# Performance work log

Hardware: AMD Instinct MI355X
Metric: run time of the kernel (lower is better)

## Reference

```python
import jax, jax.numpy as jnp
import numpy as np

NUM_EXPERTS = 64
TOP_K = 2
AUX_COEF = 0.01
Z_COEF = 0.001
INIT_STD = 0.02


def setup_inputs() -> dict:
    key = jax.random.key(0)
    k1, k2 = jax.random.split(key)
    B, S, D = 4, 4096, 2048
    x = jax.random.normal(k1, (B, S, D), dtype=jnp.float32)
    gate_w = jax.random.normal(k2, (NUM_EXPERTS, D), dtype=jnp.float32) * INIT_STD
    return {"x": x, "gate_w": gate_w}


def reference(x, gate_w):
    B, S, D = x.shape
    E, K = NUM_EXPERTS, TOP_K
    # gate linear: (B,S,D) @ (D,E) -> (B,S,E), cast to fp32 like .float()
    logits = jnp.einsum('bsd,ed->bse', x, gate_w).astype(jnp.float32)
    weights = jax.nn.softmax(logits, axis=-1)
    top_weights, top_indices = jax.lax.top_k(weights, K)
    top_weights = top_weights / jnp.sum(top_weights, axis=-1, keepdims=True)
    # load-balance aux loss (training branch)
    flat_idx = top_indices.reshape(-1)
    tokens_per_expert = jax.ops.segment_sum(
        jnp.ones_like(flat_idx, dtype=jnp.float32), flat_idx, num_segments=E)
    f = tokens_per_expert / (B * S * K)
    P = jnp.mean(weights, axis=(0, 1))
    balance_loss = E * jnp.sum(f * P)
    z_loss = jnp.mean(jnp.square(jax.nn.logsumexp(logits, axis=-1)))
    aux_loss = AUX_COEF * balance_loss + Z_COEF * z_loss
    return top_indices, top_weights, aux_loss
```

## Files before the change

kernel.cpp:

```cpp
#include <hip/hip_runtime.h>
#include <math.h>

#define NTOK 16384
#define DDIM 2048
#define NEXP 64
#define MTILE 32
#define KSUP 128
#define NSUP 16

typedef __attribute__((ext_vector_type(8))) short bf16x8;
typedef __attribute__((ext_vector_type(4))) float f32x4;

__device__ __forceinline__ unsigned short f2bf(float f) {
    unsigned int u = __builtin_bit_cast(unsigned int, f);
    u += 0x7fffu + ((u >> 16) & 1u);
    return (unsigned short)(u >> 16);
}
__device__ __forceinline__ float bf2f(unsigned short s) {
    return __builtin_bit_cast(float, ((unsigned int)s) << 16);
}
__device__ __forceinline__ void split3(float x, unsigned short &h,
                                       unsigned short &m, unsigned short &l) {
    h = f2bf(x);
    float r1 = x - bf2f(h);
    m = f2bf(r1);
    float r2 = r1 - bf2f(m);
    l = f2bf(r2);
}

__global__ void k_wpack(const float* __restrict__ gw, unsigned short* __restrict__ wp) {
    int idx = blockIdx.x * 256 + threadIdx.x;
    int lane = idx & 63;
    int ks   = (idx >> 6) & 63;
    int eg   = idx >> 12;
    int e  = eg * 16 + (lane & 15);
    int k0 = ks * 32 + (lane >> 4) * 8;
    const float* src = gw + (size_t)e * DDIM + k0;
    union { unsigned short s[8]; uint4 v; } H, M, L;
    #pragma unroll
    for (int j = 0; j < 8; ++j) split3(src[j], H.s[j], M.s[j], L.s[j]);
    size_t fb = (size_t)(eg * 64 + ks) * 1536 + lane * 8;
    *(uint4*)(wp + fb)        = H.v;
    *(uint4*)(wp + fb + 512)  = M.v;
    *(uint4*)(wp + fb + 1024) = L.v;
}

__global__ __launch_bounds__(256, 4)
void k_main(const float* __restrict__ x, const unsigned short* __restrict__ wp,
            float* __restrict__ out, float* __restrict__ gcnt,
            float* __restrict__ gP, float* __restrict__ gz) {
    __shared__ __align__(16) char As[24576];
    __shared__ float Lg[MTILE][65];
    __shared__ float Ps[NEXP], Cnt[NEXP], Zs;

    const int tid = threadIdx.x;
    if (tid < NEXP) { Ps[tid] = 0.f; Cnt[tid] = 0.f; }
    if (tid == 0) Zs = 0.f;

    const int tok0 = blockIdx.x * MTILE;
    const int lane = tid & 63;
    const int eg   = __builtin_amdgcn_readfirstlane(tid >> 6);

    const int subk = tid & 31;
    const int tokq = tid >> 5;
    const float* xbase = x + (size_t)(tok0 + tokq) * DDIM + subk * 4;

    float4 cur0 = *(const float4*)(xbase);
    float4 cur1 = *(const float4*)(xbase + 8 * DDIM);
    float4 cur2 = *(const float4*)(xbase + 16 * DDIM);
    float4 cur3 = *(const float4*)(xbase + 24 * DDIM);

    f32x4 acc0 = {0.f, 0.f, 0.f, 0.f};
    f32x4 acc1 = {0.f, 0.f, 0.f, 0.f};

    const int tau   = lane & 15;
    const int kappa = lane >> 4;

    const unsigned short* wpe = wp + (size_t)eg * 64 * 1536 + lane * 8;
    bf16x8 wf[2][3];
    #pragma unroll
    for (int p = 0; p < 3; ++p) wf[0][p] = *(const bf16x8*)(wpe + p * 512);
    #pragma unroll
    for (int p = 0; p < 3; ++p) wf[1][p] = *(const bf16x8*)(wpe + 1536 + p * 512);

    for (int ss = 0; ss < NSUP; ++ss) {
        char* bb = As;
        {
            float4 v[4] = {cur0, cur1, cur2, cur3};
            #pragma unroll
            for (int r = 0; r < 4; ++r) {
                int row = tokq + 8 * r;
                unsigned short h0,h1,h2,h3, m0,m1,m2,m3, l0,l1,l2,l3;
                split3(v[r].x, h0, m0, l0);
                split3(v[r].y, h1, m1, l1);
                split3(v[r].z, h2, m2, l2);
                split3(v[r].w, h3, m3, l3);
                uint2 H = make_uint2((unsigned)h0 | ((unsigned)h1 << 16),
                                     (unsigned)h2 | ((unsigned)h3 << 16));
                uint2 M = make_uint2((unsigned)m0 | ((unsigned)m1 << 16),
                                     (unsigned)m2 | ((unsigned)m3 << 16));
                uint2 L = make_uint2((unsigned)l0 | ((unsigned)l1 << 16),
                                     (unsigned)l2 | ((unsigned)l3 << 16));
                char* pb = bb + row * 256 + (((subk >> 1) ^ (row & 15)) << 4)
                              + (subk & 1) * 8;
                *(uint2*)(pb)         = H;
                *(uint2*)(pb + 8192)  = M;
                *(uint2*)(pb + 16384) = L;
            }
        }
        if (ss + 1 < NSUP) {
            const float* nb = xbase + (ss + 1) * KSUP;
            cur0 = *(const float4*)(nb);
            cur1 = *(const float4*)(nb + 8 * DDIM);
            cur2 = *(const float4*)(nb + 16 * DDIM);
            cur3 = *(const float4*)(nb + 24 * DDIM);
        }
        __syncthreads();
        #pragma unroll
        for (int ks = 0; ks < 4; ++ks) {
            int slotr = ((ks * 4 + kappa) ^ tau) << 4;
            const char* p0 = bb + tau * 256 + slotr;
            const char* p1 = bb + (16 + tau) * 256 + slotr;
            bf16x8 Ah0 = *(const bf16x8*)(p0);
            bf16x8 Am0 = *(const bf16x8*)(p0 + 8192);
            bf16x8 Al0 = *(const bf16x8*)(p0 + 16384);
            bf16x8 Ah1 = *(const bf16x8*)(p1);
            bf16x8 Am1 = *(const bf16x8*)(p1 + 8192);
            bf16x8 Al1 = *(const bf16x8*)(p1 + 16384);
            bf16x8 Bh = wf[ks & 1][0];
            bf16x8 Bm = wf[ks & 1][1];
            bf16x8 Bl = wf[ks & 1][2];

            acc0 = __builtin_amdgcn_mfma_f32_16x16x32_bf16(Ah0, Bh, acc0, 0, 0, 0);
            acc0 = __builtin_amdgcn_mfma_f32_16x16x32_bf16(Ah0, Bm, acc0, 0, 0, 0);
            acc0 = __builtin_amdgcn_mfma_f32_16x16x32_bf16(Am0, Bh, acc0, 0, 0, 0);
            acc0 = __builtin_amdgcn_mfma_f32_16x16x32_bf16(Ah0, Bl, acc0, 0, 0, 0);
            acc0 = __builtin_amdgcn_mfma_f32_16x16x32_bf16(Al0, Bh, acc0, 0, 0, 0);
            acc0 = __builtin_amdgcn_mfma_f32_16x16x32_bf16(Am0, Bm, acc0, 0, 0, 0);

            acc1 = __builtin_amdgcn_mfma_f32_16x16x32_bf16(Ah1, Bh, acc1, 0, 0, 0);
            acc1 = __builtin_amdgcn_mfma_f32_16x16x32_bf16(Ah1, Bm, acc1, 0, 0, 0);
            acc1 = __builtin_amdgcn_mfma_f32_16x16x32_bf16(Am1, Bh, acc1, 0, 0, 0);
            acc1 = __builtin_amdgcn_mfma_f32_16x16x32_bf16(Ah1, Bl, acc1, 0, 0, 0);
            acc1 = __builtin_amdgcn_mfma_f32_16x16x32_bf16(Al1, Bh, acc1, 0, 0, 0);
            acc1 = __builtin_amdgcn_mfma_f32_16x16x32_bf16(Am1, Bm, acc1, 0, 0, 0);

            int nk = ((ss << 2) + ks + 2) & 63;
            #pragma unroll
            for (int pI = 0; pI < 3; ++pI)
                wf[ks & 1][pI] = *(const bf16x8*)(wpe + (size_t)nk * 1536 + pI * 512);
        }
        __syncthreads();
    }

    #pragma unroll
    for (int j = 0; j < 4; ++j) {
        Lg[kappa * 4 + j][eg * 16 + tau]      = acc0[j];
        Lg[16 + kappa * 4 + j][eg * 16 + tau] = acc1[j];
    }
    __syncthreads();

    float Pacc = 0.f, zacc = 0.f;
    const int wv = tid >> 6;
    for (int i = 0; i < 8; ++i) {
        int t = wv * 8 + i;
        float l = Lg[t][lane];
        float mx = l;
        #pragma unroll
        for (int off = 32; off > 0; off >>= 1) mx = fmaxf(mx, __shfl_xor(mx, off));
        float s = expf(l - mx);
        float sum = s;
        #pragma unroll
        for (int off = 32; off > 0; off >>= 1) sum += __shfl_xor(sum, off);
        Pacc += s / sum;

        unsigned long long b1 = __ballot(l == mx);
        int i1 = __ffsll(b1) - 1;
        float l2 = (lane == i1) ? -INFINITY : l;
        float m2 = l2;
        #pragma unroll
        for (int off = 32; off > 0; off >>= 1) m2 = fmaxf(m2, __shfl_xor(m2, off));
        unsigned long long b2 = __ballot(l2 == m2);
        int i2 = __ffsll(b2) - 1;

        if (lane == 0) {
            float s2  = expf(m2 - mx);
            float inv = 1.f / (1.f + s2);
            int gt = tok0 + t;
            ((float2*)out)[gt]              = make_float2((float)i1, (float)i2);
            ((float2*)(out + 2 * NTOK))[gt] = make_float2(inv, s2 * inv);
            atomicAdd(&Cnt[i1], 1.f);
            atomicAdd(&Cnt[i2], 1.f);
            float lse = mx + logf(sum);
            zacc += lse * lse;
        }
    }
    atomicAdd(&Ps[lane], Pacc);
    if (lane == 0) atomicAdd(&Zs, zacc);
    __syncthreads();

    if (tid < NEXP) {
        atomicAdd(&gcnt[tid], Cnt[tid]);
        atomicAdd(&gP[tid],   Ps[tid]);
    }
    if (tid == 0) atomicAdd(gz, Zs);
}

__global__ void k_final(const float* __restrict__ ws, float* __restrict__ out) {
    int lane = threadIdx.x;
    float v = ws[lane] * ws[64 + lane];
    #pragma unroll
    for (int off = 32; off > 0; off >>= 1) v += __shfl_xor(v, off);
    if (lane == 0) {
        float bal = 64.f * v / (32768.f * 16384.f);
        float z   = ws[128] / 16384.f;
        out[4 * NTOK] = 0.01f * bal + 0.001f * z;
    }
}

extern "C" void kernel_launch(void* const* d_in, const int* in_sizes, int n_in,
                              void* d_out, int out_size, void* d_ws, size_t ws_size,
                              hipStream_t stream) {
    const float* x  = (const float*)d_in[0];
    const float* gw = (const float*)d_in[1];
    float* out = (float*)d_out;
    float* wsf = (float*)d_ws;
    unsigned short* wp = (unsigned short*)((char*)d_ws + 1024);

    hipMemsetAsync(d_ws, 0, 516, stream);
    k_wpack<<<64, 256, 0, stream>>>(gw, wp);
    k_main<<<NTOK / MTILE, 256, 0, stream>>>(x, wp, out, wsf, wsf + 64, wsf + 128);
    k_final<<<1, 64, 0, stream>>>(wsf, out);
}
```

Before: 84.22 us.

## Halve token tile and double-buffer split-bf16 A staging in LDS

Shrinks the per-block token tile from 32 to 16 rows, which doubles the grid size, and replaces the single LDS buffer with a double buffer. Staging the next K-chunk now overlaps with MFMA work on the current one, so only one barrier per iteration is needed instead of two. In exchange, each block reloads the full packed gate weights for only half as many tokens, which doubles weight traffic from L2, and there is less MFMA work per LDS load.

After: 86.55 us. 1.03x slower.

```diff
diff --git a/kernel.cpp b/kernel.cpp
--- a/kernel.cpp
+++ b/kernel.cpp
@@ -4,7 +4,7 @@
 #define NTOK 16384
 #define DDIM 2048
 #define NEXP 64
-#define MTILE 32
+#define MTILE 16
 #define KSUP 128
 #define NSUP 16
 
@@ -45,11 +45,27 @@
     *(uint4*)(wp + fb + 1024) = L.v;
 }
 
+__device__ __forceinline__ void stage4(char* bb, int srow, int subk, int c, float4 v) {
+    unsigned short h0,h1,h2,h3, m0,m1,m2,m3, l0,l1,l2,l3;
+    split3(v.x, h0, m0, l0);
+    split3(v.y, h1, m1, l1);
+    split3(v.z, h2, m2, l2);
+    split3(v.w, h3, m3, l3);
+    char* pb = bb + srow * 256 + (((c * 8 + (subk >> 1)) ^ srow) << 4)
+                  + (subk & 1) * 8;
+    *(uint2*)(pb)        = make_uint2((unsigned)h0 | ((unsigned)h1 << 16),
+                                      (unsigned)h2 | ((unsigned)h3 << 16));
+    *(uint2*)(pb + 4096) = make_uint2((unsigned)m0 | ((unsigned)m1 << 16),
+                                      (unsigned)m2 | ((unsigned)m3 << 16));
+    *(uint2*)(pb + 8192) = make_uint2((unsigned)l0 | ((unsigned)l1 << 16),
+                                      (unsigned)l2 | ((unsigned)l3 << 16));
+}
+
 __global__ __launch_bounds__(256, 4)
 void k_main(const float* __restrict__ x, const unsigned short* __restrict__ wp,
             float* __restrict__ out, float* __restrict__ gcnt,
             float* __restrict__ gP, float* __restrict__ gz) {
-    __shared__ __align__(16) char As[24576];
+    __shared__ __align__(16) char As[2][12288];
     __shared__ float Lg[MTILE][65];
     __shared__ float Ps[NEXP], Cnt[NEXP], Zs;
 
@@ -60,21 +76,19 @@
     const int tok0 = blockIdx.x * MTILE;
     const int lane = tid & 63;
     const int eg   = __builtin_amdgcn_readfirstlane(tid >> 6);
-
-    const int subk = tid & 31;
-    const int tokq = tid >> 5;
-    const float* xbase = x + (size_t)(tok0 + tokq) * DDIM + subk * 4;
-
-    float4 cur0 = *(const float4*)(xbase);
-    float4 cur1 = *(const float4*)(xbase + 8 * DDIM);
-    float4 cur2 = *(const float4*)(xbase + 16 * DDIM);
-    float4 cur3 = *(const float4*)(xbase + 24 * DDIM);
-
-    f32x4 acc0 = {0.f, 0.f, 0.f, 0.f};
-    f32x4 acc1 = {0.f, 0.f, 0.f, 0.f};
-
-    const int tau   = lane & 15;
+    const int tau  = lane & 15;
     const int kappa = lane >> 4;
+
+    const int srow = tid >> 4;
+    const int subk = tid & 15;
+    const float* xb = x + (size_t)(tok0 + srow) * DDIM + subk * 4;
+
+    float4 xc0 = *(const float4*)(xb);
+    float4 xc1 = *(const float4*)(xb + 64);
+    stage4(As[0], srow, subk, 0, xc0);
+    stage4(As[0], srow, subk, 1, xc1);
+    xc0 = *(const float4*)(xb + 128);
+    xc1 = *(const float4*)(xb + 128 + 64);
 
     const unsigned short* wpe = wp + (size_t)eg * 64 * 1536 + lane * 8;
     bf16x8 wf[2][3];
@@ -83,87 +97,52 @@
     #pragma unroll
     for (int p = 0; p < 3; ++p) wf[1][p] = *(const bf16x8*)(wpe + 1536 + p * 512);
 
+    f32x4 acc = {0.f, 0.f, 0.f, 0.f};
+
     for (int ss = 0; ss < NSUP; ++ss) {
-        char* bb = As;
-        {
-            float4 v[4] = {cur0, cur1, cur2, cur3};
-            #pragma unroll
-            for (int r = 0; r < 4; ++r) {
-                int row = tokq + 8 * r;
-                unsigned short h0,h1,h2,h3, m0,m1,m2,m3, l0,l1,l2,l3;
-                split3(v[r].x, h0, m0, l0);
-                split3(v[r].y, h1, m1, l1);
-                split3(v[r].z, h2, m2, l2);
-                split3(v[r].w, h3, m3, l3);
-                uint2 H = make_uint2((unsigned)h0 | ((unsigned)h1 << 16),
-                                     (unsigned)h2 | ((unsigned)h3 << 16));
-                uint2 M = make_uint2((unsigned)m0 | ((unsigned)m1 << 16),
-                                     (unsigned)m2 | ((unsigned)m3 << 16));
-                uint2 L = make_uint2((unsigned)l0 | ((unsigned)l1 << 16),
-                                     (unsigned)l2 | ((unsigned)l3 << 16));
-                char* pb = bb + row * 256 + (((subk >> 1) ^ (row & 15)) << 4)
-                              + (subk & 1) * 8;
-                *(uint2*)(pb)         = H;
-                *(uint2*)(pb + 8192)  = M;
-                *(uint2*)(pb + 16384) = L;
-            }
+        __syncthreads();
+        if (ss + 1 < NSUP) {
+            char* nb = As[(ss + 1) & 1];
+            stage4(nb, srow, subk, 0, xc0);
+            stage4(nb, srow, subk, 1, xc1);
+            int nss = (ss + 2) & (NSUP - 1);
+            xc0 = *(const float4*)(xb + nss * KSUP);
+            xc1 = *(const float4*)(xb + nss * KSUP + 64);
         }
-        if (ss + 1 < NSUP) {
-            const float* nb = xbase + (ss + 1) * KSUP;
-            cur0 = *(const float4*)(nb);
-            cur1 = *(const float4*)(nb + 8 * DDIM);
-            cur2 = *(const float4*)(nb + 16 * DDIM);
-            cur3 = *(const float4*)(nb + 24 * DDIM);
-        }
-        __syncthreads();
+        const char* bb = As[ss & 1];
         #pragma unroll
         for (int ks = 0; ks < 4; ++ks) {
-            int slotr = ((ks * 4 + kappa) ^ tau) << 4;
-            const char* p0 = bb + tau * 256 + slotr;
-            const char* p1 = bb + (16 + tau) * 256 + slotr;
-            bf16x8 Ah0 = *(const bf16x8*)(p0);
-            bf16x8 Am0 = *(const bf16x8*)(p0 + 8192);
-            bf16x8 Al0 = *(const bf16x8*)(p0 + 16384);
-            bf16x8 Ah1 = *(const bf16x8*)(p1);
-            bf16x8 Am1 = *(const bf16x8*)(p1 + 8192);
-            bf16x8 Al1 = *(const bf16x8*)(p1 + 16384);
+            const char* p0 = bb + tau * 256 + ((((ks << 2) + kappa) ^ tau) << 4);
+            bf16x8 Ah = *(const bf16x8*)(p0);
+            bf16x8 Am = *(const bf16x8*)(p0 + 4096);
+            bf16x8 Al = *(const bf16x8*)(p0 + 8192);
             bf16x8 Bh = wf[ks & 1][0];
             bf16x8 Bm = wf[ks & 1][1];
             bf16x8 Bl = wf[ks & 1][2];
 
-            acc0 = __builtin_amdgcn_mfma_f32_16x16x32_bf16(Ah0, Bh, acc0, 0, 0, 0);
-            acc0 = __builtin_amdgcn_mfma_f32_16x16x32_bf16(Ah0, Bm, acc0, 0, 0, 0);
-            acc0 = __builtin_amdgcn_mfma_f32_16x16x32_bf16(Am0, Bh, acc0, 0, 0, 0);
-            acc0 = __builtin_amdgcn_mfma_f32_16x16x32_bf16(Ah0, Bl, acc0, 0, 0, 0);
-            acc0 = __builtin_amdgcn_mfma_f32_16x16x32_bf16(Al0, Bh, acc0, 0, 0, 0);
-            acc0 = __builtin_amdgcn_mfma_f32_16x16x32_bf16(Am0, Bm, acc0, 0, 0, 0);
-
-            acc1 = __builtin_amdgcn_mfma_f32_16x16x32_bf16(Ah1, Bh, acc1, 0, 0, 0);
-            acc1 = __builtin_amdgcn_mfma_f32_16x16x32_bf16(Ah1, Bm, acc1, 0, 0, 0);
-            acc1 = __builtin_amdgcn_mfma_f32_16x16x32_bf16(Am1, Bh, acc1, 0, 0, 0);
-            acc1 = __builtin_amdgcn_mfma_f32_16x16x32_bf16(Ah1, Bl, acc1, 0, 0, 0);
-            acc1 = __builtin_amdgcn_mfma_f32_16x16x32_bf16(Al1, Bh, acc1, 0, 0, 0);
-            acc1 = __builtin_amdgcn_mfma_f32_16x16x32_bf16(Am1, Bm, acc1, 0, 0, 0);
+            acc = __builtin_amdgcn_mfma_f32_16x16x32_bf16(Ah, Bh, acc, 0, 0, 0);
+            acc = __builtin_amdgcn_mfma_f32_16x16x32_bf16(Ah, Bm, acc, 0, 0, 0);
+            acc = __builtin_amdgcn_mfma_f32_16x16x32_bf16(Am, Bh, acc, 0, 0, 0);
+            acc = __builtin_amdgcn_mfma_f32_16x16x32_bf16(Ah, Bl, acc, 0, 0, 0);
+            acc = __builtin_amdgcn_mfma_f32_16x16x32_bf16(Al, Bh, acc, 0, 0, 0);
+            acc = __builtin_amdgcn_mfma_f32_16x16x32_bf16(Am, Bm, acc, 0, 0, 0);
 
             int nk = ((ss << 2) + ks + 2) & 63;
             #pragma unroll
             for (int pI = 0; pI < 3; ++pI)
                 wf[ks & 1][pI] = *(const bf16x8*)(wpe + (size_t)nk * 1536 + pI * 512);
         }
-        __syncthreads();
-    }
-
-    #pragma unroll
-    for (int j = 0; j < 4; ++j) {
-        Lg[kappa * 4 + j][eg * 16 + tau]      = acc0[j];
-        Lg[16 + kappa * 4 + j][eg * 16 + tau] = acc1[j];
-    }
+    }
+
+    #pragma unroll
+    for (int j = 0; j < 4; ++j)
+        Lg[kappa * 4 + j][eg * 16 + tau] = acc[j];
     __syncthreads();
 
     float Pacc = 0.f, zacc = 0.f;
     const int wv = tid >> 6;
-    for (int i = 0; i < 8; ++i) {
-        int t = wv * 8 + i;
+    for (int i = 0; i < 4; ++i) {
+        int t = wv * 4 + i;
         float l = Lg[t][lane];
         float mx = l;
         #pragma unroll
```
